# Kernel tuning notes

Measured on AMD Instinct MI355X. Metric: run time of the kernel, lower is better.

The kernel has to match this reference:

```python
import jax, jax.numpy as jnp
import numpy as np

DIST_THRESHOLD = 0.001
DIST_COEFF = 10000.0
BOX_CENTER = np.array([-0.001782, 1.005e-05, 0.0431621], dtype=np.float32)
HALF_EXT = np.array([0.204416 / 2 + DIST_THRESHOLD,
                     0.0632517 / 2 + DIST_THRESHOLD,
                     0.1381738 / 2 + DIST_THRESHOLD], dtype=np.float32)


def _qmul(a, b):
    # Hamilton product, quaternions stored as [x, y, z, w] (scipy convention used by the repo)
    av, aw = a[..., :3], a[..., 3:]
    bv, bw = b[..., :3], b[..., 3:]
    w = aw * bw - jnp.sum(av * bv, axis=-1, keepdims=True)
    v = aw * bv + bw * av + jnp.cross(av, bv)
    return jnp.concatenate([v, w], axis=-1)


def _qconj(q):
    return jnp.concatenate([-q[..., :3], q[..., 3:]], axis=-1)


def _qinv(q):
    return _qconj(q) / jnp.sum(q * q, axis=-1, keepdims=True)


def setup_inputs() -> dict:
    key = jax.random.key(0)
    k1, k2, k3 = jax.random.split(key, 3)
    B, N = 4096, 4096
    trans = jax.random.normal(k1, (B, 3), dtype=jnp.float32) * 0.05
    quat = jax.random.normal(k2, (B, 4), dtype=jnp.float32)
    quat = quat / jnp.linalg.norm(quat, axis=-1, keepdims=True)
    pc = jax.random.normal(k3, (B, N, 3), dtype=jnp.float32) * 0.1
    return {"trans": trans, "quat": quat, "pc": pc}


def reference(trans, quat, pc):
    # rotate pc by inverse quaternion: q_inv * p * conj(q_inv)
    qi = _qinv(quat)[:, None, :]                       # [B,1,4]
    p4 = jnp.concatenate([pc, jnp.zeros_like(pc[..., :1])], axis=-1)  # [B,N,4]
    pc_rot = _qmul(_qmul(qi, p4), _qconj(qi))[..., :3]  # [B,N,3]
    pc_t = pc_rot - trans[:, None, :]

    # axis-aligned bbox mask
    lo = jnp.asarray(BOX_CENTER - HALF_EXT)
    hi = jnp.asarray(BOX_CENTER + HALF_EXT)
    mask = jnp.all((pc_t >= lo) & (pc_t <= hi), axis=-1)  # [B,N]

    # per-batch masked mean of point norms (vectorized segment reduce)
    norms = jnp.linalg.norm(pc_t, axis=-1)              # [B,N]
    cnt = jnp.sum(mask, axis=-1)                         # [B]
    s = jnp.sum(jnp.where(mask, norms, 0.0), axis=-1)    # [B]
    dist = jnp.where(cnt > 0, -s / jnp.maximum(cnt, 1).astype(norms.dtype), 1.0)
    return dist[:, None] * DIST_COEFF
```

## Files before the change

kernel.cpp:

```cpp
#include <hip/hip_runtime.h>
#include <hip/hip_bf16.h>


#define DIST_COEFF 10000.0f

__global__ __launch_bounds__(256) void collision_dist_kernel(
    const float* __restrict__ trans,
    const float* __restrict__ quat,
    const float* __restrict__ pc,
    float* __restrict__ out,
    int N)
{
    const int b = blockIdx.x;

    const float qx = quat[b * 4 + 0];
    const float qy = quat[b * 4 + 1];
    const float qz = quat[b * 4 + 2];
    const float qw = quat[b * 4 + 3];
    const float n2 = qx * qx + qy * qy + qz * qz + qw * qw;
    const float inv = 1.0f / n2;
    const float ax = -qx * inv;
    const float ay = -qy * inv;
    const float az = -qz * inv;
    const float aw =  qw * inv;

    const float tx = trans[b * 3 + 0];
    const float ty = trans[b * 3 + 1];
    const float tz = trans[b * 3 + 2];

    const float cx = -0.001782f, cy = 1.005e-05f, cz = 0.0431621f;
    const float hx = 0.204416f * 0.5f + 0.001f;
    const float hy = 0.0632517f * 0.5f + 0.001f;
    const float hz = 0.1381738f * 0.5f + 0.001f;
    const float lox = cx - hx, hix = cx + hx;
    const float loy = cy - hy, hiy = cy + hy;
    const float loz = cz - hz, hiz = cz + hz;

    const float* row = pc + (size_t)b * (size_t)N * 3u;

    float s = 0.0f;
    int cnt = 0;

    auto point = [&](float px, float py, float pz) {
        const float w1  = -(ax * px + ay * py + az * pz);
        const float v1x = aw * px + (ay * pz - az * py);
        const float v1y = aw * py + (az * px - ax * pz);
        const float v1z = aw * pz + (ax * py - ay * px);
        const float rx = -w1 * ax + aw * v1x - (v1y * az - v1z * ay);
        const float ry = -w1 * ay + aw * v1y - (v1z * ax - v1x * az);
        const float rz = -w1 * az + aw * v1z - (v1x * ay - v1y * ax);
        const float fx = rx - tx;
        const float fy = ry - ty;
        const float fz = rz - tz;
        const bool inside = (fx >= lox) & (fx <= hix) &
                            (fy >= loy) & (fy <= hiy) &
                            (fz >= loz) & (fz <= hiz);
        if (inside) {
            cnt += 1;
            s += sqrtf(fx * fx + fy * fy + fz * fz);
        }
    };

    const int nchunk = N >> 2;
    const float4* row4 = reinterpret_cast<const float4*>(row);
    for (int c = threadIdx.x; c < nchunk; c += blockDim.x) {
        const float4 v0 = row4[c * 3 + 0];
        const float4 v1 = row4[c * 3 + 1];
        const float4 v2 = row4[c * 3 + 2];
        point(v0.x, v0.y, v0.z);
        point(v0.w, v1.x, v1.y);
        point(v1.z, v1.w, v2.x);
        point(v2.y, v2.z, v2.w);
    }
    for (int i = (nchunk << 2) + threadIdx.x; i < N; i += blockDim.x) {
        point(row[i * 3 + 0], row[i * 3 + 1], row[i * 3 + 2]);
    }

    float fc = (float)cnt;
    #pragma unroll
    for (int off = 32; off > 0; off >>= 1) {
        s  += __shfl_down(s, off, 64);
        fc += __shfl_down(fc, off, 64);
    }

    __shared__ float ss[8];
    __shared__ float sc[8];
    const int lane = threadIdx.x & 63;
    const int wid  = threadIdx.x >> 6;
    if (lane == 0) { ss[wid] = s; sc[wid] = fc; }
    __syncthreads();
    if (threadIdx.x == 0) {
        float S = 0.0f, C = 0.0f;
        const int nw = (blockDim.x + 63) >> 6;
        for (int w = 0; w < nw; ++w) { S += ss[w]; C += sc[w]; }
        const float dist = (C > 0.0f) ? (-S / C) : 1.0f;
        out[b] = dist * DIST_COEFF;
    }
}

extern "C" void kernel_launch(void* const* d_in, const int* in_sizes, int n_in,
                              void* d_out, int out_size, void* d_ws, size_t ws_size,
                              hipStream_t stream) {
    const float* trans = (const float*)d_in[0];
    const float* quat  = (const float*)d_in[1];
    const float* pc    = (const float*)d_in[2];
    float* out = (float*)d_out;

    const int B = in_sizes[0] / 3;
    const int N = (int)((long long)in_sizes[2] / (3LL * B));

    collision_dist_kernel<<<B, 256, 0, stream>>>(trans, quat, pc, out, N);
}
```

Baseline: 278.2 us.

## Stage point chunks into LDS via global_load_lds and use rotation matrix

Adds a staged kernel that copies 1024-point chunks of the point cloud straight into shared memory with direct global-to-LDS loads. Each thread then reads its xyz from LDS and transforms it with a precomputed 3x3 rotation matrix in FMAs instead of two quaternion products. The masked accumulation becomes branch-free. The chunk loop has no double buffering, so the two barriers per chunk may leave memory latency exposed on a bandwidth-bound stream. A generic fallback kernel handles N that is not a multiple of 1024.

```diff
diff --git a/kernel.cpp b/kernel.cpp
--- a/kernel.cpp
+++ b/kernel.cpp
@@ -1,28 +1,39 @@
 #include <hip/hip_runtime.h>
 #include <hip/hip_bf16.h>
 
-
 #define DIST_COEFF 10000.0f
 
-__global__ __launch_bounds__(256) void collision_dist_kernel(
+#define AS1(p) ((__attribute__((address_space(1))) void*)(p))
+#define AS3(p) ((__attribute__((address_space(3))) void*)(p))
+
+__global__ __launch_bounds__(256) void collision_dist_staged(
     const float* __restrict__ trans,
     const float* __restrict__ quat,
     const float* __restrict__ pc,
     float* __restrict__ out,
     int N)
 {
-    const int b = blockIdx.x;
+    const int b    = blockIdx.x;
+    const int tid  = threadIdx.x;
+    const int w    = tid >> 6;
+    const int lane = tid & 63;
 
     const float qx = quat[b * 4 + 0];
     const float qy = quat[b * 4 + 1];
     const float qz = quat[b * 4 + 2];
     const float qw = quat[b * 4 + 3];
-    const float n2 = qx * qx + qy * qy + qz * qz + qw * qw;
-    const float inv = 1.0f / n2;
-    const float ax = -qx * inv;
-    const float ay = -qy * inv;
-    const float az = -qz * inv;
-    const float aw =  qw * inv;
+    const float inv = 1.0f / (qx * qx + qy * qy + qz * qz + qw * qw);
+    const float ax = -qx * inv, ay = -qy * inv, az = -qz * inv, aw = qw * inv;
+    const float d = aw * aw - (ax * ax + ay * ay + az * az);
+    const float m00 = d + 2.0f * ax * ax;
+    const float m01 = 2.0f * ax * ay - 2.0f * aw * az;
+    const float m02 = 2.0f * ax * az + 2.0f * aw * ay;
+    const float m10 = 2.0f * ay * ax + 2.0f * aw * az;
+    const float m11 = d + 2.0f * ay * ay;
+    const float m12 = 2.0f * ay * az - 2.0f * aw * ax;
+    const float m20 = 2.0f * az * ax - 2.0f * aw * ay;
+    const float m21 = 2.0f * az * ay + 2.0f * aw * ax;
+    const float m22 = d + 2.0f * az * az;
 
     const float tx = trans[b * 3 + 0];
     const float ty = trans[b * 3 + 1];
@@ -36,65 +47,118 @@
     const float loy = cy - hy, hiy = cy + hy;
     const float loz = cz - hz, hiz = cz + hz;
 
+    __shared__ float lds[3072];
+
+    const float* rowp  = pc + (size_t)b * (size_t)N * 3u;
+    const float4* row4 = reinterpret_cast<const float4*>(rowp);
+
+    const int nchunk = N >> 10;
+    float s = 0.0f, c = 0.0f;
+
+    for (int ck = 0; ck < nchunk; ++ck) {
+        const float4* g4 = row4 + (size_t)ck * 768u;
+        #pragma unroll
+        for (int j = 0; j < 3; ++j) {
+            __builtin_amdgcn_global_load_lds(
+                AS1(g4 + j * 256 + tid),
+                AS3(lds + (j * 256 + w * 64) * 4),
+                16, 0, 0);
+        }
+        __syncthreads();
+
+        #pragma unroll
+        for (int r = 0; r < 4; ++r) {
+            const int p = r * 256 + tid;
+            const float px = lds[3 * p + 0];
+            const float py = lds[3 * p + 1];
+            const float pz = lds[3 * p + 2];
+            const float fx = fmaf(m00, px, fmaf(m01, py, fmaf(m02, pz, -tx)));
+            const float fy = fmaf(m10, px, fmaf(m11, py, fmaf(m12, pz, -ty)));
+            const float fz = fmaf(m20, px, fmaf(m21, py, fmaf(m22, pz, -tz)));
+            const bool inside = (fx >= lox) & (fx <= hix) &
+                                (fy >= loy) & (fy <= hiy) &
+                                (fz >= loz) & (fz <= hiz);
+            const float nrm = sqrtf(fmaf(fx, fx, fmaf(fy, fy, fz * fz)));
+            s += inside ? nrm : 0.0f;
+            c += inside ? 1.0f : 0.0f;
+        }
+        __syncthreads();
+    }
+
+    #pragma unroll
+    for (int off = 32; off > 0; off >>= 1) {
+        s += __shfl_down(s, off, 64);
+        c += __shfl_down(c, off, 64);
+    }
+
+    __shared__ float rs[4], rc[4];
+    if (lane == 0) { rs[w] = s; rc[w] = c; }
+    __syncthreads();
+    if (tid == 0) {
+        const float S = rs[0] + rs[1] + rs[2] + rs[3];
+        const float C = rc[0] + rc[1] + rc[2] + rc[3];
+        const float dist = (C > 0.0f) ? (-S / C) : 1.0f;
+        out[b] = dist * DIST_COEFF;
+    }
+}
+
+__global__ __launch_bounds__(256) void collision_dist_generic(
+    const float* __restrict__ trans,
+    const float* __restrict__ quat,
+    const float* __restrict__ pc,
+    float* __restrict__ out,
+    int N)
+{
+    const int b = blockIdx.x;
+    const float qx = quat[b * 4 + 0], qy = quat[b * 4 + 1];
+    const float qz = quat[b * 4 + 2], qw = quat[b * 4 + 3];
+    const float inv = 1.0f / (qx * qx + qy * qy + qz * qz + qw * qw);
+    const float ax = -qx * inv, ay = -qy * inv, az = -qz * inv, aw = qw * inv;
+    const float tx = trans[b * 3 + 0], ty = trans[b * 3 + 1], tz = trans[b * 3 + 2];
+
+    const float cx = -0.001782f, cy = 1.005e-05f, cz = 0.0431621f;
+    const float hx = 0.204416f * 0.5f + 0.001f;
+    const float hy = 0.0632517f * 0.5f + 0.001f;
+    const float hz = 0.1381738f * 0.5f + 0.001f;
+    const float lox = cx - hx, hix = cx + hx;
+    const float loy = cy - hy, hiy = cy + hy;
+    const float loz = cz - hz, hiz = cz + hz;
+
     const float* row = pc + (size_t)b * (size_t)N * 3u;
+    float s = 0.0f, c = 0.0f;
 
-    float s = 0.0f;
-    int cnt = 0;
-
-    auto point = [&](float px, float py, float pz) {
+    for (int i = threadIdx.x; i < N; i += blockDim.x) {
+        const float px = row[i * 3 + 0];
+        const float py = row[i * 3 + 1];
+        const float pz = row[i * 3 + 2];
         const float w1  = -(ax * px + ay * py + az * pz);
         const float v1x = aw * px + (ay * pz - az * py);
         const float v1y = aw * py + (az * px - ax * pz);
         const float v1z = aw * pz + (ax * py - ay * px);
-        const float rx = -w1 * ax + aw * v1x - (v1y * az - v1z * ay);
-        const float ry = -w1 * ay + aw * v1y - (v1z * ax - v1x * az);
-        const float rz = -w1 * az + aw * v1z - (v1x * ay - v1y * ax);
-        const float fx = rx - tx;
-        const float fy = ry - ty;
-        const float fz = rz - tz;
+        const float fx = -w1 * ax + aw * v1x - (v1y * az - v1z * ay) - tx;
+        const float fy = -w1 * ay + aw * v1y - (v1z * ax - v1x * az) - ty;
+        const float fz = -w1 * az + aw * v1z - (v1x * ay - v1y * ax) - tz;
         const bool inside = (fx >= lox) & (fx <= hix) &
                             (fy >= loy) & (fy <= hiy) &
                             (fz >= loz) & (fz <= hiz);
-        if (inside) {
-            cnt += 1;
-            s += sqrtf(fx * fx + fy * fy + fz * fz);
-        }
-    };
-
-    const int nchunk = N >> 2;
-    const float4* row4 = reinterpret_cast<const float4*>(row);
-    for (int c = threadIdx.x; c < nchunk; c += blockDim.x) {
-        const float4 v0 = row4[c * 3 + 0];
-        const float4 v1 = row4[c * 3 + 1];
-        const float4 v2 = row4[c * 3 + 2];
-        point(v0.x, v0.y, v0.z);
-        point(v0.w, v1.x, v1.y);
-        point(v1.z, v1.w, v2.x);
-        point(v2.y, v2.z, v2.w);
-    }
-    for (int i = (nchunk << 2) + threadIdx.x; i < N; i += blockDim.x) {
-        point(row[i * 3 + 0], row[i * 3 + 1], row[i * 3 + 2]);
+        const float nrm = sqrtf(fx * fx + fy * fy + fz * fz);
+        s += inside ? nrm : 0.0f;
+        c += inside ? 1.0f : 0.0f;
     }
 
-    float fc = (float)cnt;
     #pragma unroll
     for (int off = 32; off > 0; off >>= 1) {
-        s  += __shfl_down(s, off, 64);
-        fc += __shfl_down(fc, off, 64);
+        s += __shfl_down(s, off, 64);
+        c += __shfl_down(c, off, 64);
     }
-
-    __shared__ float ss[8];
-    __shared__ float sc[8];
-    const int lane = threadIdx.x & 63;
-    const int wid  = threadIdx.x >> 6;
-    if (lane == 0) { ss[wid] = s; sc[wid] = fc; }
+    __shared__ float rs[4], rc[4];
+    const int lane = threadIdx.x & 63, w = threadIdx.x >> 6;
+    if (lane == 0) { rs[w] = s; rc[w] = c; }
     __syncthreads();
     if (threadIdx.x == 0) {
         float S = 0.0f, C = 0.0f;
-        const int nw = (blockDim.x + 63) >> 6;
-        for (int w = 0; w < nw; ++w) { S += ss[w]; C += sc[w]; }
-        const float dist = (C > 0.0f) ? (-S / C) : 1.0f;
-        out[b] = dist * DIST_COEFF;
+        for (int i = 0; i < 4; ++i) { S += rs[i]; C += rc[i]; }
+        out[b] = ((C > 0.0f) ? (-S / C) : 1.0f) * DIST_COEFF;
     }
 }
 
@@ -109,5 +173,9 @@
     const int B = in_sizes[0] / 3;
     const int N = (int)((long long)in_sizes[2] / (3LL * B));
 
-    collision_dist_kernel<<<B, 256, 0, stream>>>(trans, quat, pc, out, N);
+    if ((N & 1023) == 0) {
+        collision_dist_staged<<<B, 256, 0, stream>>>(trans, quat, pc, out, N);
+    } else {
+        collision_dist_generic<<<B, 256, 0, stream>>>(trans, quat, pc, out, N);
+    }
 }
```

New measurement: 277.3 us. Within noise of the previous version (-0.3%).
